# Kernel optimization log

Hardware: AMD Instinct MI355X
Metric: run time of the kernel (lower is better)

Reference implementation:

```python
import jax, jax.numpy as jnp
import numpy as np

N, H, W, D, K = 32, 36, 36, 512, 64
POOL = 3  # pool_list=[3] -> 3x3 grid of regions
EPS = 1e-12


def setup_inputs() -> dict:
    key = jax.random.key(0)
    k1, k2, k3 = jax.random.split(key, 3)
    x = jax.random.normal(k1, (N, H, W, D), dtype=jnp.float32)
    W_conv = jax.random.normal(k2, (D, K), dtype=jnp.float32) * 0.05
    C = jax.random.normal(k3, (D, K), dtype=jnp.float32) * 0.05
    return {"x": x, "W_conv": W_conv, "C": C}


def _l2norm(v, axis):
    return v / jnp.sqrt(jnp.sum(v * v, axis=axis, keepdims=True) + EPS)


def _encode_vlad(xm, W_conv, C):
    # xm: [N, h, w, D]
    s = jnp.einsum('nhwd,dk->nhwk', xm, W_conv)          # 1x1 conv, no bias
    a = jax.nn.softmax(s, axis=-1)                        # soft assignment [N,h,w,K]
    # Faithful to sum_hw a * (x[...,None] - C) without the [N,h,w,D,K] blow-up:
    # = einsum(x, a) - C * sum_hw(a)
    asum = jnp.sum(a, axis=(1, 2))                        # [N, K]
    v = jnp.einsum('nhwd,nhwk->ndk', xm, a) - C[None] * asum[:, None, :]  # [N, D, K]
    # intra-normalization: normalize each cluster's residual over D
    v = _l2norm(v, axis=1)                                # [N, D, K]
    v = v.reshape(v.shape[0], -1)                         # flatten (row-major, matches tf)
    v = _l2norm(v, axis=-1)                               # [N, D*K]
    return v


def reference(x, W_conv, C):
    n, h, w, d = x.shape
    rl, cl = h / POOL, w / POOL
    outs = []
    for jy in range(POOL):
        for ix in range(POOL):
            y1, y2 = int(round(jy * rl)), int(round(jy * rl + rl))
            x1, x2 = int(round(ix * cl)), int(round(ix * cl + cl))
            outs.append(_encode_vlad(x[:, y1:y2, x1:x2, :], W_conv, C))
    return jnp.concatenate(outs, axis=1)  # [N, POOL*POOL*D*K]
```

## Files before the change

kernel.cpp:

```cpp
#include <hip/hip_runtime.h>

typedef __attribute__((ext_vector_type(4))) float f32x4;
typedef __attribute__((ext_vector_type(8))) short short8;

#define EPSF 1e-12f

__device__ __forceinline__ ushort bf16rne(float x) {
  uint u = __float_as_uint(x);
  u += 0x7fffu + ((u >> 16) & 1u);
  return (ushort)(u >> 16);
}
__device__ __forceinline__ float bf2f(ushort h) {
  return __uint_as_float(((uint)h) << 16);
}
__device__ __forceinline__ f32x4 mfma16(short8 a, short8 b, f32x4 c) {
  return __builtin_amdgcn_mfma_f32_16x16x32_bf16(a, b, c, 0, 0, 0);
}

__global__ __launch_bounds__(256) void k0_wt(const float* __restrict__ W,
                                             ushort* __restrict__ ws2) {
  int k = blockIdx.x;
  int mi = k >> 4, l15k = k & 15;
  for (int task = threadIdx.x; task < 512; task += 256) {
    int dg8 = task >> 3, j = task & 7;
    int d = dg8 * 8 + j;
    int s2 = dg8 >> 2, hi16d = dg8 & 3;
    int l = hi16d * 16 + l15k;
    float v = W[(size_t)d * 64 + k];
    ushort h = bf16rne(v);
    size_t idx = ((size_t)(s2 * 4 + mi) * 64 + l) * 8 + j;
    ws2[idx] = h;
    ws2[32768 + idx] = bf16rne(v - bf2f(h));
  }
}

__global__ __launch_bounds__(256, 6) void k1_assign(
    const float* __restrict__ x, const ushort* __restrict__ ws2,
    ushort* __restrict__ aTu, float* __restrict__ asum_ws) {
  __shared__ char sm[25472];
  ushort* xH = (ushort*)sm;
  ushort* xL = (ushort*)(sm + 12480);
  float* smax = (float*)(sm + 24960);
  float* ssum = (float*)(sm + 25216);

  int b = blockIdx.x;
  int n = b / 108, rem = b % 108;
  int y = rem / 3, col = rem % 3;
  int t = threadIdx.x;
  int w = t >> 6, lane = t & 63, l15 = lane & 15, hi16 = lane >> 4;
  const float4* xb4 =
      (const float4*)(x + ((size_t)n * 1296 + y * 36 + col * 12) * 512);

  float4 stg[6];
#pragma unroll
  for (int i = 0; i < 6; ++i) stg[i] = xb4[t + i * 256];
#pragma unroll
  for (int i = 0; i < 6; ++i) {
    int idx = t + i * 256;
    int p = idx >> 7, q = idx & 127;
    int gp = (q >> 1) ^ (p & 7);
    int off = p * 520 + gp * 8 + (q & 1) * 4;
    float4 v = stg[i];
    ushort h0 = bf16rne(v.x), h1 = bf16rne(v.y), h2 = bf16rne(v.z), h3 = bf16rne(v.w);
    uint2 hp, lp;
    hp.x = (uint)h0 | ((uint)h1 << 16);
    hp.y = (uint)h2 | ((uint)h3 << 16);
    lp.x = (uint)bf16rne(v.x - bf2f(h0)) | ((uint)bf16rne(v.y - bf2f(h1)) << 16);
    lp.y = (uint)bf16rne(v.z - bf2f(h2)) | ((uint)bf16rne(v.w - bf2f(h3)) << 16);
    *(uint2*)(xH + off) = hp;
    *(uint2*)(xL + off) = lp;
  }
  __syncthreads();

  int pr = (l15 < 12) ? l15 : 0;
  f32x4 acc = (f32x4){0.f, 0.f, 0.f, 0.f};
#pragma unroll
  for (int s = 0; s < 16; ++s) {
    const ushort* aPtr = ws2 + ((size_t)(s * 4 + w) * 64 + lane) * 8;
    short8 aH = *(const short8*)aPtr;
    short8 aL = *(const short8*)(aPtr + 32768);
    int g = s * 4 + hi16;
    const ushort* bp = xH + pr * 520 + ((g ^ (pr & 7)) << 3);
    short8 bH = *(const short8*)bp;
    short8 bL = *(const short8*)(bp + 6240);
    acc = mfma16(aH, bH, acc);
    acc = mfma16(aH, bL, acc);
    acc = mfma16(aL, bH, acc);
  }

  {
    float m = fmaxf(fmaxf(acc[0], acc[1]), fmaxf(acc[2], acc[3]));
    m = fmaxf(m, __shfl_xor(m, 16));
    m = fmaxf(m, __shfl_xor(m, 32));
    if (hi16 == 0) smax[w * 16 + l15] = m;
  }
  __syncthreads();
  float e[4];
  {
    float M = fmaxf(fmaxf(smax[0 * 16 + l15], smax[1 * 16 + l15]),
                    fmaxf(smax[2 * 16 + l15], smax[3 * 16 + l15]));
    float s = 0.f;
#pragma unroll
    for (int rr = 0; rr < 4; ++rr) {
      e[rr] = __expf(acc[rr] - M);
      s += e[rr];
    }
    s += __shfl_xor(s, 16);
    s += __shfl_xor(s, 32);
    if (hi16 == 0) ssum[w * 16 + l15] = s;
  }
  __syncthreads();
  float S = ssum[0 * 16 + l15] + ssum[1 * 16 + l15] + ssum[2 * 16 + l15] +
            ssum[3 * 16 + l15];
  float inv = 1.f / S;

  int region = n * 9 + (y / 12) * 3 + col;
  int prow = y % 12;
  size_t slot = (size_t)region * 19456;
  float av[4];
#pragma unroll
  for (int rr = 0; rr < 4; ++rr) {
    float a = (l15 < 12) ? e[rr] * inv : 0.f;
    av[rr] = a;
    float s = a;
    s += __shfl_xor(s, 1);
    s += __shfl_xor(s, 2);
    s += __shfl_xor(s, 4);
    s += __shfl_xor(s, 8);
    if (l15 == 0) asum_ws[(size_t)b * 64 + w * 16 + hi16 * 4 + rr] = s;
  }
  if (l15 < 12) {
#pragma unroll
    for (int rr = 0; rr < 4; ++rr) {
      int k = w * 16 + hi16 * 4 + rr;
      ushort h = bf16rne(av[rr]);
      aTu[slot + (size_t)k * 152 + prow * 12 + l15] = h;
      aTu[slot + 9728 + (size_t)k * 152 + prow * 12 + l15] =
          bf16rne(av[rr] - bf2f(h));
    }
  }
  if (prow == 11 && col == 2) {
    int plane = t >> 7, kk = (t >> 1) & 63, half = t & 1;
    uint2 z; z.x = 0u; z.y = 0u;
    *(uint2*)(aTu + slot + (size_t)plane * 9728 + (size_t)kk * 152 + 144 + half * 4) = z;
  }
}

__global__ __launch_bounds__(512, 8) void k2_vlad(
    const float* __restrict__ x, const float* __restrict__ C,
    const float4* __restrict__ aT_ws, const float* __restrict__ asum_ws,
    float* __restrict__ out, float* __restrict__ colnorm) {
  __shared__ float4 smv[2504];
  char* sm = (char*)smv;
  ushort* atH = (ushort*)sm;
  ushort* atL = (ushort*)(sm + 19456);
  int* poff = (int*)(sm + 38912);
  float* asumS = (float*)(sm + 39552);
  float* cn2 = (float*)(sm + 39808);

  int b = blockIdx.x;
  int reg = b % 288;
  int dc = b / 288;
  int n = reg / 9, r = reg % 9;
  int d0 = dc * 64;
  int y1 = (r / 3) * 12, x1 = (r % 3) * 12;
  int t = threadIdx.x;
  int w = t >> 6, lane = t & 63, l15 = lane & 15, hi16 = lane >> 4;
  const float* xn = x + (size_t)n * (36 * 36 * 512);

  if (t < 160) poff[t] = (t < 144) ? ((y1 + t / 12) * 36 + (x1 + t % 12)) * 512 : 0;
  if (t < 64) {
    int ry = r / 3, rc = r % 3;
    float s = 0.f;
#pragma unroll
    for (int j = 0; j < 12; ++j)
      s += asum_ws[(size_t)(n * 108 + (ry * 12 + j) * 3 + rc) * 64 + t];
    asumS[t] = s;
    cn2[t] = 0.f;
  }
  {
    const float4* src = aT_ws + (size_t)reg * 2432;
    for (int i = t; i < 2432; i += 512) smv[i] = src[i];
  }
  __syncthreads();

  int mi = w & 3, kh = w >> 2;
  int drow = d0 + mi * 16 + l15;
  const float* xcol = xn + drow;

  f32x4 acc[2];
  acc[0] = (f32x4){0.f, 0.f, 0.f, 0.f};
  acc[1] = (f32x4){0.f, 0.f, 0.f, 0.f};

#pragma unroll
  for (int ks = 0; ks < 5; ++ks) {
    int pb = ks * 32 + hi16 * 8;
    int4 poA = *reinterpret_cast<const int4*>(&poff[pb]);
    int4 poB = *reinterpret_cast<const int4*>(&poff[pb + 4]);
    float av[8];
    av[0] = xcol[poA.x]; av[1] = xcol[poA.y];
    av[2] = xcol[poA.z]; av[3] = xcol[poA.w];
    av[4] = xcol[poB.x]; av[5] = xcol[poB.y];
    av[6] = xcol[poB.z]; av[7] = xcol[poB.w];
    bool valid = (ks < 4) || (hi16 < 2);
    short8 ah, al;
#pragma unroll
    for (int j = 0; j < 8; ++j) {
      float v = valid ? av[j] : 0.f;
      ushort h = bf16rne(v);
      ah[j] = (short)h;
      al[j] = (short)bf16rne(v - bf2f(h));
    }
#pragma unroll
    for (int ni = 0; ni < 2; ++ni) {
      int row = kh * 32 + ni * 16 + l15;
      short8 bh = *(const short8*)(atH + row * 152 + pb);
      short8 bl = *(const short8*)(atL + row * 152 + pb);
      f32x4 a0 = acc[ni];
      a0 = mfma16(ah, bh, a0);
      a0 = mfma16(ah, bl, a0);
      a0 = mfma16(al, bh, a0);
      acc[ni] = a0;
    }
  }

  size_t obase = (size_t)reg * (512 * 64);
#pragma unroll
  for (int ni = 0; ni < 2; ++ni) {
    int k = kh * 32 + ni * 16 + l15;
    float ak = asumS[k];
    float s2 = 0.f;
#pragma unroll
    for (int rr = 0; rr < 4; ++rr) {
      int d = d0 + mi * 16 + hi16 * 4 + rr;
      float v = acc[ni][rr] - C[(size_t)d * 64 + k] * ak;
      out[obase + (size_t)d * 64 + k] = v;
      s2 += v * v;
    }
    atomicAdd(&cn2[k], s2);
  }
  __syncthreads();
  if (t < 64) colnorm[(size_t)(reg * 8 + dc) * 64 + t] = cn2[t];
}

__global__ __launch_bounds__(256) void k3_scale(float* __restrict__ out,
                                                const float* __restrict__ colnorm) {
  int b = blockIdx.x;
  int reg = b % 288;
  int dc = b / 288;

  __shared__ float ratio[64];
  __shared__ float fs[64];
  int t = threadIdx.x;
  float c = 0.f;
  if (t < 64) {
#pragma unroll
    for (int j = 0; j < 8; ++j) c += colnorm[(size_t)(reg * 8 + j) * 64 + t];
    ratio[t] = c / (c + EPSF);
  }
  __syncthreads();
  if (t < 64) {
    float g = 0.f;
#pragma unroll
    for (int j = 0; j < 64; ++j) g += ratio[j];
    fs[t] = rsqrtf(c + EPSF) * rsqrtf(g + EPSF);
  }
  __syncthreads();

  size_t base4 = (((size_t)reg * 512) + (size_t)dc * 128) * 64 / 4;
  float4* o4 = reinterpret_cast<float4*>(out);
  for (int j = 0; j < 8; ++j) {
    size_t idx = base4 + t + 256 * j;
    float4 v = o4[idx];
    int k0 = (int)((idx * 4) & 63);
    v.x *= fs[k0]; v.y *= fs[k0 + 1]; v.z *= fs[k0 + 2]; v.w *= fs[k0 + 3];
    o4[idx] = v;
  }
}

extern "C" void kernel_launch(void* const* d_in, const int* in_sizes, int n_in,
                              void* d_out, int out_size, void* d_ws, size_t ws_size,
                              hipStream_t stream) {
  const float* x = (const float*)d_in[0];
  const float* Wc = (const float*)d_in[1];
  const float* C = (const float*)d_in[2];
  float* out = (float*)d_out;

  char* ws = (char*)d_ws;
  ushort* ws2 = (ushort*)(ws);
  float* asum_ws = (float*)(ws + 131072);
  float* colnorm = (float*)(ws + 1015808);
  char* aT_base = ws + 1605632;

  k0_wt<<<64, 256, 0, stream>>>(Wc, ws2);
  k1_assign<<<3456, 256, 0, stream>>>(x, ws2, (ushort*)aT_base, asum_ws);
  k2_vlad<<<2304, 512, 0, stream>>>(x, C, (const float4*)aT_base, asum_ws, out, colnorm);
  k3_scale<<<1152, 256, 0, stream>>>(out, colnorm);
}
```

Baseline: 92.91 us.

## Stage soft-assignment tile in LDS and write coalesced, transpose in k2 load

```diff
diff --git a/kernel.cpp b/kernel.cpp
--- a/kernel.cpp
+++ b/kernel.cpp
@@ -37,11 +37,12 @@
 __global__ __launch_bounds__(256, 6) void k1_assign(
     const float* __restrict__ x, const ushort* __restrict__ ws2,
     ushort* __restrict__ aTu, float* __restrict__ asum_ws) {
-  __shared__ char sm[25472];
+  __shared__ char sm[25664];
   ushort* xH = (ushort*)sm;
-  ushort* xL = (ushort*)(sm + 12480);
-  float* smax = (float*)(sm + 24960);
-  float* ssum = (float*)(sm + 25216);
+  ushort* xL = (ushort*)(sm + 12576);
+  ushort* aStage = (ushort*)sm;
+  float* smax = (float*)(sm + 25152);
+  float* ssum = (float*)(sm + 25408);
 
   int b = blockIdx.x;
   int n = b / 108, rem = b % 108;
@@ -59,7 +60,7 @@
     int idx = t + i * 256;
     int p = idx >> 7, q = idx & 127;
     int gp = (q >> 1) ^ (p & 7);
-    int off = p * 520 + gp * 8 + (q & 1) * 4;
+    int off = p * 524 + gp * 8 + (q & 1) * 4;
     float4 v = stg[i];
     ushort h0 = bf16rne(v.x), h1 = bf16rne(v.y), h2 = bf16rne(v.z), h3 = bf16rne(v.w);
     uint2 hp, lp;
@@ -72,7 +73,7 @@
   }
   __syncthreads();
 
-  int pr = (l15 < 12) ? l15 : 0;
+  int pr = (l15 < 12) ? l15 : (l15 - 12);
   f32x4 acc = (f32x4){0.f, 0.f, 0.f, 0.f};
 #pragma unroll
   for (int s = 0; s < 16; ++s) {
@@ -80,9 +81,9 @@
     short8 aH = *(const short8*)aPtr;
     short8 aL = *(const short8*)(aPtr + 32768);
     int g = s * 4 + hi16;
-    const ushort* bp = xH + pr * 520 + ((g ^ (pr & 7)) << 3);
+    const ushort* bp = xH + pr * 524 + ((g ^ (pr & 7)) << 3);
     short8 bH = *(const short8*)bp;
-    short8 bL = *(const short8*)(bp + 6240);
+    short8 bL = *(const short8*)(bp + 12576 / 2);
     acc = mfma16(aH, bH, acc);
     acc = mfma16(aH, bL, acc);
     acc = mfma16(aL, bH, acc);
@@ -114,41 +115,35 @@
             ssum[3 * 16 + l15];
   float inv = 1.f / S;
 
-  int region = n * 9 + (y / 12) * 3 + col;
-  int prow = y % 12;
-  size_t slot = (size_t)region * 19456;
-  float av[4];
 #pragma unroll
   for (int rr = 0; rr < 4; ++rr) {
     float a = (l15 < 12) ? e[rr] * inv : 0.f;
-    av[rr] = a;
+    int k = w * 16 + hi16 * 4 + rr;
     float s = a;
     s += __shfl_xor(s, 1);
     s += __shfl_xor(s, 2);
     s += __shfl_xor(s, 4);
     s += __shfl_xor(s, 8);
-    if (l15 == 0) asum_ws[(size_t)b * 64 + w * 16 + hi16 * 4 + rr] = s;
-  }
-  if (l15 < 12) {
-#pragma unroll
-    for (int rr = 0; rr < 4; ++rr) {
-      int k = w * 16 + hi16 * 4 + rr;
-      ushort h = bf16rne(av[rr]);
-      aTu[slot + (size_t)k * 152 + prow * 12 + l15] = h;
-      aTu[slot + 9728 + (size_t)k * 152 + prow * 12 + l15] =
-          bf16rne(av[rr] - bf2f(h));
-    }
-  }
-  if (prow == 11 && col == 2) {
-    int plane = t >> 7, kk = (t >> 1) & 63, half = t & 1;
-    uint2 z; z.x = 0u; z.y = 0u;
-    *(uint2*)(aTu + slot + (size_t)plane * 9728 + (size_t)kk * 152 + 144 + half * 4) = z;
+    if (l15 == 0) asum_ws[(size_t)b * 64 + k] = s;
+    if (l15 < 12) {
+      ushort h = bf16rne(a);
+      aStage[k * 12 + l15] = h;
+      aStage[768 + k * 12 + l15] = bf16rne(a - bf2f(h));
+    }
+  }
+  __syncthreads();
+
+  if (t < 192) {
+    float4 v = ((const float4*)aStage)[t];
+    float4* dst = (float4*)(aTu + (size_t)(n * 9 + (y / 12) * 3 + col) * 18432 +
+                            (size_t)(y % 12) * 1536);
+    dst[t] = v;
   }
 }
 
 __global__ __launch_bounds__(512, 8) void k2_vlad(
     const float* __restrict__ x, const float* __restrict__ C,
-    const float4* __restrict__ aT_ws, const float* __restrict__ asum_ws,
+    const ushort* __restrict__ aTu, const float* __restrict__ asum_ws,
     float* __restrict__ out, float* __restrict__ colnorm) {
   __shared__ float4 smv[2504];
   char* sm = (char*)smv;
@@ -179,8 +174,23 @@
     cn2[t] = 0.f;
   }
   {
-    const float4* src = aT_ws + (size_t)reg * 2432;
-    for (int i = t; i < 2432; i += 512) smv[i] = src[i];
+    const uint2* src = (const uint2*)(aTu + (size_t)reg * 18432);
+#pragma unroll
+    for (int i = 0; i < 9; ++i) {
+      int tau = t + i * 512;
+      uint2 v = src[tau];
+      int row = tau / 384;
+      int rm = tau - row * 384;
+      int plane = rm / 192;
+      int rm2 = rm - plane * 192;
+      int k = rm2 / 3, c = rm2 - k * 3;
+      *(uint2*)(sm + plane * 19456 + k * 304 + row * 24 + c * 8) = v;
+    }
+    if (t < 256) {
+      int plane = t >> 7, k = (t >> 1) & 63, h = t & 1;
+      uint2 z; z.x = 0u; z.y = 0u;
+      *(uint2*)(sm + plane * 19456 + k * 304 + 288 + h * 8) = z;
+    }
   }
   __syncthreads();
 
@@ -294,6 +304,6 @@
 
   k0_wt<<<64, 256, 0, stream>>>(Wc, ws2);
   k1_assign<<<3456, 256, 0, stream>>>(x, ws2, (ushort*)aT_base, asum_ws);
-  k2_vlad<<<2304, 512, 0, stream>>>(x, C, (const float4*)aT_base, asum_ws, out, colnorm);
+  k2_vlad<<<2304, 512, 0, stream>>>(x, C, (const ushort*)aT_base, asum_ws, out, colnorm);
   k3_scale<<<1152, 256, 0, stream>>>(out, colnorm);
 }
```

Result: slower. 116.3 us (+25.1%).
